# Optimization experiments

Hardware: AMD Instinct MI355X
Metric: run time of the kernel (lower is better)

The kernel has to match this reference:

```python
import jax, jax.numpy as jnp
import numpy as np


def setup_inputs() -> dict:
    key = jax.random.key(0)
    k1, k2, k3, k4 = jax.random.split(key, 4)
    T = 64            # decoder_batch_len (target steps)
    B = 32            # batch_size
    V = 50257         # decoder vocab size
    L = 400           # encoder (source) length
    rows = T * B
    vocab_ds = jax.random.uniform(k1, (rows, V), dtype=jnp.float32)
    attns = jax.random.uniform(k2, (rows, L), dtype=jnp.float32)
    p_gens = jax.random.uniform(k3, (rows, 1), dtype=jnp.float32)
    sources = jax.random.randint(k4, (L, B), 0, V, dtype=jnp.int64)
    return {
        "vocab_ds": vocab_ds,
        "attns": attns,
        "p_gens": p_gens,
        "sources": sources,
        "decoder_batch_len": T,
    }


def reference(vocab_ds, attns, p_gens, sources, decoder_batch_len):
    # vocab_ds: (T*B, V), attns: (T*B, L), p_gens: (T*B, 1), sources: (L, B)
    rows, V = vocab_ds.shape
    vocab_dists = p_gens * vocab_ds                      # gated generation dist
    attn_dists = (1.0 - p_gens) * attns                  # gated copy dist
    # sources.T tiled over decoder steps -> per-row vocab ids, shape (T*B, L)
    sources_rep = jnp.tile(sources.T, (decoder_batch_len, 1))
    row_idx = jnp.arange(rows)[:, None]                  # (T*B, 1) broadcasts over L
    # torch scatter_ (overwrite semantics) of copy probs into vocab slots
    attn_dists_projected = jnp.zeros((rows, V), dtype=vocab_ds.dtype).at[
        row_idx, sources_rep
    ].set(attn_dists, mode="drop")
    final_dists = attn_dists_projected + vocab_dists
    return final_dists
```

## Files before the change

### kernel.cpp

```cpp
#include <hip/hip_runtime.h>

typedef float f32x4 __attribute__((ext_vector_type(4)));
typedef unsigned int uint32;

#define MAXV 51200
#define NWMAX (MAXV / 32 + 1)
#define LPAD 1024

__global__ __launch_bounds__(256) void sort_kernel(
    const int* __restrict__ sources, int* __restrict__ sv, int* __restrict__ sl,
    int L, int B, int V)
{
    const int b = blockIdx.x;
    __shared__ int s_col[LPAD];
    for (int l = threadIdx.x; l < L; l += 256) {
        const int v = sources[(size_t)l * B + b];
        s_col[l] = (v >= 0 && v < V) ? v : 0x7FFFFFFF;
    }
    __syncthreads();
    int* __restrict__ svb = sv + (size_t)b * L;
    int* __restrict__ slb = sl + (size_t)b * L;
    for (int l = threadIdx.x; l < L; l += 256) {
        const int v = s_col[l];
        int rank = 0;
        for (int k = 0; k < L; ++k) {
            const int vk = s_col[k];
            rank += (vk < v) || (vk == v && k < l);
        }
        svb[rank] = v;
        slb[rank] = l;
    }
}

__global__ __launch_bounds__(256) void fused_kernel(
    const float* __restrict__ vd, const float* __restrict__ attns,
    const float* __restrict__ pgs, const int* __restrict__ sv,
    const int* __restrict__ sl, float* __restrict__ out, int V, int L, int B)
{
    const int row = blockIdx.x;
    const int tid = threadIdx.x;
    const int b   = row % B;

    __shared__ uint32 bm[NWMAX];
    __shared__ int    s_v[LPAD];
    __shared__ int    s_l[LPAD];
    __shared__ float  s_attn[LPAD];

    const int NW = (V + 31) >> 5;
    for (int w = tid; w < NW + 1; w += 256) bm[w] = 0u;
    const int* __restrict__ svb = sv + (size_t)b * L;
    const int* __restrict__ slb = sl + (size_t)b * L;
    for (int t = tid; t < LPAD; t += 256) {
        s_v[t]    = (t < L) ? svb[t] : 0x7FFFFFFF;
        s_l[t]    = (t < L) ? slb[t] : 0;
        s_attn[t] = (t < L) ? attns[(size_t)row * L + t] : 0.0f;
    }
    __syncthreads();
    for (int t = tid; t < L; t += 256) {
        const int v = s_v[t];
        if (v < V) atomicOr(&bm[v >> 5], 1u << (v & 31));
    }
    __syncthreads();

    const float pg   = pgs[row];
    const float gate = 1.0f - pg;
    const size_t base = (size_t)row * (size_t)V;

    auto lookup = [&](int j) -> float {
        int lo = 0, hi = LPAD;
        while (lo < hi) {
            const int mid = (lo + hi) >> 1;
            if (s_v[mid] <= j) lo = mid + 1; else hi = mid;
        }
        return gate * s_attn[s_l[lo - 1]];
    };

    const int mis  = (int)(base & 3);
    const int pre  = mis ? (4 - mis) : 0;
    const int preN = pre < V ? pre : V;
    if (tid < preN) {
        const int j = tid;
        float x = pg * vd[base + j];
        if ((bm[j >> 5] >> (j & 31)) & 1u) x += lookup(j);
        __builtin_nontemporal_store(x, &out[base + j]);
    }

    const int nvec = (V - preN) >> 2;
    const f32x4* __restrict__ v4 = (const f32x4*)(vd + base + preN);
    f32x4* __restrict__ o4       = (f32x4*)(out + base + preN);

    auto proc = [&](int i) {
        f32x4 x = v4[i];
        x *= pg;
        const int j0 = preN + (i << 2);
        const int w  = j0 >> 5;
        const uint32 sh = (uint32)(j0 & 31);
        uint32 bits;
        if (sh <= 28u) bits = (bm[w] >> sh) & 0xFu;
        else           bits = ((bm[w] >> sh) | (bm[w + 1] << (32u - sh))) & 0xFu;
        if (bits) {
#pragma unroll
            for (int e = 0; e < 4; ++e)
                if ((bits >> e) & 1u) x[e] += lookup(j0 + e);
        }
        __builtin_nontemporal_store(x, &o4[i]);
    };

    int i = tid;
    for (; i + 768 < nvec; i += 1024) {
        proc(i); proc(i + 256); proc(i + 512); proc(i + 768);
    }
    for (; i < nvec; i += 256) proc(i);

    for (int j = preN + (nvec << 2) + tid; j < V; j += 256) {
        float x = pg * vd[base + j];
        if ((bm[j >> 5] >> (j & 31)) & 1u) x += lookup(j);
        __builtin_nontemporal_store(x, &out[base + j]);
    }
}

__global__ __launch_bounds__(256) void fused_fallback_kernel(
    const float* __restrict__ vocab_ds, const float* __restrict__ attns,
    const float* __restrict__ p_gens, const int* __restrict__ sources,
    float* __restrict__ out, int V, int L, int B)
{
    const int row = blockIdx.x;
    const int tid = threadIdx.x;
    const size_t base = (size_t)row * (size_t)V;
    const float pg = p_gens[row];

    const int mis  = (int)(base & 3);
    const int pre  = mis ? (4 - mis) : 0;
    const int preN = pre < V ? pre : V;
    for (int j = tid; j < preN; j += blockDim.x)
        out[base + j] = pg * vocab_ds[base + j];
    const int nvec = (V - preN) >> 2;
    const f32x4* __restrict__ v4 = (const f32x4*)(vocab_ds + base + preN);
    f32x4* __restrict__ o4       = (f32x4*)(out + base + preN);
    for (int i = tid; i < nvec; i += blockDim.x) {
        f32x4 x = v4[i];
        x *= pg;
        o4[i] = x;
    }
    for (int j = preN + (nvec << 2) + tid; j < V; j += blockDim.x)
        out[base + j] = pg * vocab_ds[base + j];

    __shared__ int s_src[512];
    const int b = row % B;
    const bool use_lds = (L <= 512);
    if (use_lds) {
        for (int l = tid; l < L; l += blockDim.x)
            s_src[l] = sources[(size_t)l * B + b];
    }
    __syncthreads();
    const float gate = 1.0f - pg;
    for (int l = tid; l < L; l += blockDim.x) {
        const int v = use_lds ? s_src[l] : sources[(size_t)l * B + b];
        if (v < 0 || v >= V) continue;
        bool last = true;
        for (int l2 = l + 1; l2 < L; ++l2) {
            const int v2 = use_lds ? s_src[l2] : sources[(size_t)l2 * B + b];
            if (v2 == v) { last = false; break; }
        }
        if (last) {
            const float a = gate * attns[(size_t)row * L + l];
            out[base + v] = pg * vocab_ds[base + v] + a;
        }
    }
}

extern "C" void kernel_launch(void* const* d_in, const int* in_sizes, int n_in,
                              void* d_out, int out_size, void* d_ws, size_t ws_size,
                              hipStream_t stream) {
    const float* vocab_ds = (const float*)d_in[0];
    const float* attns    = (const float*)d_in[1];
    const float* p_gens   = (const float*)d_in[2];
    const int*   sources  = (const int*)d_in[3];
    const int rows = in_sizes[2];
    const int V    = in_sizes[0] / rows;
    const int L    = in_sizes[1] / rows;
    const int B    = in_sizes[3] / L;
    float* out = (float*)d_out;

    const size_t need = (size_t)B * (size_t)L * 2 * sizeof(int);
    const bool fits = (ws_size >= need) && (V <= (NWMAX - 1) * 32) && (L <= LPAD);
    if (fits) {
        int* sv = (int*)d_ws;
        int* sl = sv + (size_t)B * (size_t)L;
        sort_kernel<<<B, 256, 0, stream>>>(sources, sv, sl, L, B, V);
        fused_kernel<<<rows, 256, 0, stream>>>(vocab_ds, attns, p_gens,
                                               sv, sl, out, V, L, B);
    } else {
        fused_fallback_kernel<<<rows, 256, 0, stream>>>(
            vocab_ds, attns, p_gens, sources, out, V, L, B);
    }
}
```

Before: 234.4 us.

## Flatten main kernel into grid-stride loop with global per-batch bitmaps

```diff
diff --git a/kernel.cpp b/kernel.cpp
--- a/kernel.cpp
+++ b/kernel.cpp
@@ -2,22 +2,25 @@
 
 typedef float f32x4 __attribute__((ext_vector_type(4)));
 typedef unsigned int uint32;
-
-#define MAXV 51200
-#define NWMAX (MAXV / 32 + 1)
+typedef unsigned long long uint64;
+
 #define LPAD 1024
 
-__global__ __launch_bounds__(256) void sort_kernel(
+__global__ __launch_bounds__(256) void prep_kernel(
     const int* __restrict__ sources, int* __restrict__ sv, int* __restrict__ sl,
-    int L, int B, int V)
+    uint32* __restrict__ bmG, int L, int B, int V, int NWp)
 {
     const int b = blockIdx.x;
+    uint32* __restrict__ bmb = bmG + (size_t)b * NWp;
+    for (int w = threadIdx.x; w < NWp; w += 256) bmb[w] = 0u;
+
     __shared__ int s_col[LPAD];
     for (int l = threadIdx.x; l < L; l += 256) {
         const int v = sources[(size_t)l * B + b];
         s_col[l] = (v >= 0 && v < V) ? v : 0x7FFFFFFF;
     }
     __syncthreads();
+
     int* __restrict__ svb = sv + (size_t)b * L;
     int* __restrict__ slb = sl + (size_t)b * L;
     for (int l = threadIdx.x; l < L; l += 256) {
@@ -29,93 +32,98 @@
         }
         svb[rank] = v;
         slb[rank] = l;
-    }
-}
-
-__global__ __launch_bounds__(256) void fused_kernel(
+        if (v < V) atomicOr(&bmb[v >> 5], 1u << (v & 31));
+    }
+}
+
+__global__ __launch_bounds__(256) void fused_flat_kernel(
     const float* __restrict__ vd, const float* __restrict__ attns,
     const float* __restrict__ pgs, const int* __restrict__ sv,
-    const int* __restrict__ sl, float* __restrict__ out, int V, int L, int B)
+    const int* __restrict__ sl, const uint32* __restrict__ bmG,
+    float* __restrict__ out, int V, int L, int B, int NWp,
+    uint64 magicM, long long n4, long long total)
 {
-    const int row = blockIdx.x;
-    const int tid = threadIdx.x;
-    const int b   = row % B;
-
-    __shared__ uint32 bm[NWMAX];
-    __shared__ int    s_v[LPAD];
-    __shared__ int    s_l[LPAD];
-    __shared__ float  s_attn[LPAD];
-
-    const int NW = (V + 31) >> 5;
-    for (int w = tid; w < NW + 1; w += 256) bm[w] = 0u;
-    const int* __restrict__ svb = sv + (size_t)b * L;
-    const int* __restrict__ slb = sl + (size_t)b * L;
-    for (int t = tid; t < LPAD; t += 256) {
-        s_v[t]    = (t < L) ? svb[t] : 0x7FFFFFFF;
-        s_l[t]    = (t < L) ? slb[t] : 0;
-        s_attn[t] = (t < L) ? attns[(size_t)row * L + t] : 0.0f;
-    }
-    __syncthreads();
-    for (int t = tid; t < L; t += 256) {
-        const int v = s_v[t];
-        if (v < V) atomicOr(&bm[v >> 5], 1u << (v & 31));
-    }
-    __syncthreads();
-
-    const float pg   = pgs[row];
-    const float gate = 1.0f - pg;
-    const size_t base = (size_t)row * (size_t)V;
-
-    auto lookup = [&](int j) -> float {
-        int lo = 0, hi = LPAD;
-        while (lo < hi) {
-            const int mid = (lo + hi) >> 1;
-            if (s_v[mid] <= j) lo = mid + 1; else hi = mid;
-        }
-        return gate * s_attn[s_l[lo - 1]];
-    };
-
-    const int mis  = (int)(base & 3);
-    const int pre  = mis ? (4 - mis) : 0;
-    const int preN = pre < V ? pre : V;
-    if (tid < preN) {
-        const int j = tid;
-        float x = pg * vd[base + j];
-        if ((bm[j >> 5] >> (j & 31)) & 1u) x += lookup(j);
-        __builtin_nontemporal_store(x, &out[base + j]);
-    }
-
-    const int nvec = (V - preN) >> 2;
-    const f32x4* __restrict__ v4 = (const f32x4*)(vd + base + preN);
-    f32x4* __restrict__ o4       = (f32x4*)(out + base + preN);
-
-    auto proc = [&](int i) {
-        f32x4 x = v4[i];
-        x *= pg;
-        const int j0 = preN + (i << 2);
-        const int w  = j0 >> 5;
-        const uint32 sh = (uint32)(j0 & 31);
-        uint32 bits;
-        if (sh <= 28u) bits = (bm[w] >> sh) & 0xFu;
-        else           bits = ((bm[w] >> sh) | (bm[w + 1] << (32u - sh))) & 0xFu;
-        if (bits) {
+    const long long stride = (long long)gridDim.x * 256;
+    const uint32 bpow2 = ((B & (B - 1)) == 0);
+
+    for (long long i4 = (long long)blockIdx.x * 256 + threadIdx.x;
+         i4 < n4; i4 += stride) {
+        const uint64 g0 = (uint64)i4 << 2;
+        uint32 row = (uint32)((g0 * magicM) >> 48);
+        uint32 j0  = (uint32)(g0 - (uint64)row * (uint32)V);
+        f32x4 x = *(const f32x4*)(vd + g0);
+
+        if (j0 + 4u <= (uint32)V) {
+            const float pg = pgs[row];
+            x *= pg;
+            const uint32 b = bpow2 ? (row & (uint32)(B - 1)) : (row % (uint32)B);
+            const uint32* __restrict__ bmb = bmG + (size_t)b * NWp;
+            const uint32 w = j0 >> 5, sh = j0 & 31u;
+            uint32 bits = bmb[w] >> sh;
+            if (sh > 28u) bits |= bmb[w + 1] << (32u - sh);
+            bits &= 0xFu;
+            if (bits) {
+                const float gate = 1.0f - pg;
+                const int* __restrict__ svb = sv + (size_t)b * L;
+                const int* __restrict__ slb = sl + (size_t)b * L;
 #pragma unroll
-            for (int e = 0; e < 4; ++e)
-                if ((bits >> e) & 1u) x[e] += lookup(j0 + e);
-        }
-        __builtin_nontemporal_store(x, &o4[i]);
-    };
-
-    int i = tid;
-    for (; i + 768 < nvec; i += 1024) {
-        proc(i); proc(i + 256); proc(i + 512); proc(i + 768);
-    }
-    for (; i < nvec; i += 256) proc(i);
-
-    for (int j = preN + (nvec << 2) + tid; j < V; j += 256) {
-        float x = pg * vd[base + j];
-        if ((bm[j >> 5] >> (j & 31)) & 1u) x += lookup(j);
-        __builtin_nontemporal_store(x, &out[base + j]);
+                for (int e = 0; e < 4; ++e)
+                    if ((bits >> e) & 1u) {
+                        const int j = (int)(j0 + e);
+                        int lo = 0, hi = L;
+                        while (lo < hi) {
+                            const int mid = (lo + hi) >> 1;
+                            if (svb[mid] <= j) lo = mid + 1; else hi = mid;
+                        }
+                        x[e] += gate * attns[(size_t)row * L + slb[lo - 1]];
+                    }
+            }
+            __builtin_nontemporal_store(x, (f32x4*)(out + g0));
+        } else {
+            f32x4 xo;
+#pragma unroll
+            for (int e = 0; e < 4; ++e) {
+                uint32 re = row, je = j0 + e;
+                if (je >= (uint32)V) { re = row + 1; je -= (uint32)V; }
+                const float pg = pgs[re];
+                float xe = x[e] * pg;
+                const uint32 b = bpow2 ? (re & (uint32)(B - 1)) : (re % (uint32)B);
+                const uint32* __restrict__ bmb = bmG + (size_t)b * NWp;
+                if ((bmb[je >> 5] >> (je & 31u)) & 1u) {
+                    const int* __restrict__ svb = sv + (size_t)b * L;
+                    const int* __restrict__ slb = sl + (size_t)b * L;
+                    int lo = 0, hi = L;
+                    while (lo < hi) {
+                        const int mid = (lo + hi) >> 1;
+                        if (svb[mid] <= (int)je) lo = mid + 1; else hi = mid;
+                    }
+                    xe += (1.0f - pg) * attns[(size_t)re * L + slb[lo - 1]];
+                }
+                xo[e] = xe;
+            }
+            __builtin_nontemporal_store(xo, (f32x4*)(out + g0));
+        }
+    }
+
+    for (long long g = (n4 << 2) + (long long)blockIdx.x * 256 + threadIdx.x;
+         g < total; g += stride) {
+        const uint32 row = (uint32)(((uint64)g * magicM) >> 48);
+        const uint32 j   = (uint32)((uint64)g - (uint64)row * (uint32)V);
+        const float pg = pgs[row];
+        float xe = pg * vd[g];
+        const uint32 b = bpow2 ? (row & (uint32)(B - 1)) : (row % (uint32)B);
+        const uint32* bmb = bmG + (size_t)b * NWp;
+        if ((bmb[j >> 5] >> (j & 31u)) & 1u) {
+            const int* svb = sv + (size_t)b * L;
+            const int* slb = sl + (size_t)b * L;
+            int lo = 0, hi = L;
+            while (lo < hi) {
+                const int mid = (lo + hi) >> 1;
+                if (svb[mid] <= (int)j) lo = mid + 1; else hi = mid;
+            }
+            xe += (1.0f - pg) * attns[(size_t)row * L + slb[lo - 1]];
+        }
+        __builtin_nontemporal_store(xe, &out[g]);
     }
 }
 
@@ -182,14 +190,25 @@
     const int B    = in_sizes[3] / L;
     float* out = (float*)d_out;
 
-    const size_t need = (size_t)B * (size_t)L * 2 * sizeof(int);
-    const bool fits = (ws_size >= need) && (V <= (NWMAX - 1) * 32) && (L <= LPAD);
+    const int NWp = ((V + 31) >> 5) + 1;
+    const size_t need = (size_t)B * (size_t)L * 2 * sizeof(int)
+                      + (size_t)B * (size_t)NWp * sizeof(uint32);
+    const bool fits = (ws_size >= need) && (L <= LPAD);
+
     if (fits) {
-        int* sv = (int*)d_ws;
-        int* sl = sv + (size_t)B * (size_t)L;
-        sort_kernel<<<B, 256, 0, stream>>>(sources, sv, sl, L, B, V);
-        fused_kernel<<<rows, 256, 0, stream>>>(vocab_ds, attns, p_gens,
-                                               sv, sl, out, V, L, B);
+        int*    sv  = (int*)d_ws;
+        int*    sl  = sv + (size_t)B * (size_t)L;
+        uint32* bmG = (uint32*)(sl + (size_t)B * (size_t)L);
+
+        const long long total = (long long)rows * (long long)V;
+        const long long n4    = total >> 2;
+        const uint64 magicM =
+            (uint64)((((__uint128_t)1) << 48) / (uint32)V) + 1ull;
+
+        prep_kernel<<<B, 256, 0, stream>>>(sources, sv, sl, bmG, L, B, V, NWp);
+        fused_flat_kernel<<<2048, 256, 0, stream>>>(
+            vocab_ds, attns, p_gens, sv, sl, bmG, out,
+            V, L, B, NWp, magicM, n4, total);
     } else {
         fused_fallback_kernel<<<rows, 256, 0, stream>>>(
             vocab_ds, attns, p_gens, sources, out, V, L, B);
```

Measured after the change: 481.7 us. 106% more time.

## Software-pipeline vocab loads with inline-asm loads and explicit vmcnt waits

Applied to the files above, without the earlier changes.

```diff
diff --git a/kernel.cpp b/kernel.cpp
--- a/kernel.cpp
+++ b/kernel.cpp
@@ -89,28 +89,66 @@
     const f32x4* __restrict__ v4 = (const f32x4*)(vd + base + preN);
     f32x4* __restrict__ o4       = (f32x4*)(out + base + preN);
 
-    auto proc = [&](int i) {
-        f32x4 x = v4[i];
+    auto finish = [&](f32x4 x, int i, f32x4* po) {
         x *= pg;
         const int j0 = preN + (i << 2);
         const int w  = j0 >> 5;
         const uint32 sh = (uint32)(j0 & 31);
-        uint32 bits;
-        if (sh <= 28u) bits = (bm[w] >> sh) & 0xFu;
-        else           bits = ((bm[w] >> sh) | (bm[w + 1] << (32u - sh))) & 0xFu;
+        uint32 bits = bm[w] >> sh;
+        if (sh > 28u) bits |= bm[w + 1] << (32u - sh);
+        bits &= 0xFu;
         if (bits) {
 #pragma unroll
             for (int e = 0; e < 4; ++e)
                 if ((bits >> e) & 1u) x[e] += lookup(j0 + e);
         }
-        __builtin_nontemporal_store(x, &o4[i]);
+        __builtin_nontemporal_store(x, po);
     };
 
-    int i = tid;
-    for (; i + 768 < nvec; i += 1024) {
-        proc(i); proc(i + 256); proc(i + 512); proc(i + 768);
-    }
-    for (; i < nvec; i += 256) proc(i);
+    const int nfull  = nvec >> 8;
+    int nppipe = nfull & ~7;
+
+    if (nppipe >= 8) {
+        const f32x4* pl = v4 + tid;
+        f32x4*       po = o4 + tid;
+        int icur = tid;
+        f32x4 x0, x1, x2, x3, x4_, x5, x6, x7;
+
+#define LOADV(xx)                                                         \
+        asm volatile("global_load_dwordx4 %0, %1, off"                    \
+                     : "=&v"(xx) : "v"(pl) : "memory");                   \
+        pl += 256;
+
+#define CONSUME(xx)                                                       \
+        asm volatile("s_waitcnt vmcnt(7)" ::: "memory");                  \
+        __builtin_amdgcn_sched_barrier(0);                                \
+        finish(xx, icur, po);                                             \
+        po += 256; icur += 256;
+
+        LOADV(x0) LOADV(x1) LOADV(x2) LOADV(x3)
+        LOADV(x4_) LOADV(x5) LOADV(x6) LOADV(x7)
+
+        const int trips = nppipe - 8;
+        for (int t = 0; t < trips; t += 8) {
+            CONSUME(x0) LOADV(x0)
+            CONSUME(x1) LOADV(x1)
+            CONSUME(x2) LOADV(x2)
+            CONSUME(x3) LOADV(x3)
+            CONSUME(x4_) LOADV(x4_)
+            CONSUME(x5) LOADV(x5)
+            CONSUME(x6) LOADV(x6)
+            CONSUME(x7) LOADV(x7)
+        }
+        CONSUME(x0) CONSUME(x1) CONSUME(x2) CONSUME(x3)
+        CONSUME(x4_) CONSUME(x5) CONSUME(x6) CONSUME(x7)
+#undef LOADV
+#undef CONSUME
+    } else {
+        nppipe = 0;
+    }
+
+    for (int i = nppipe * 256 + tid; i < nvec; i += 256)
+        finish(v4[i], i, o4 + i);
 
     for (int j = preN + (nvec << 2) + tid; j < V; j += 256) {
         float x = pg * vd[base + j];
```

New measurement: 251.4 us. 1.07x slower.

## Stream vocab rows through LDS with double-buffered global_load_lds pipeline

Applied to the files above, without the earlier changes.

```diff
diff --git a/kernel.cpp b/kernel.cpp
--- a/kernel.cpp
+++ b/kernel.cpp
@@ -2,10 +2,13 @@
 
 typedef float f32x4 __attribute__((ext_vector_type(4)));
 typedef unsigned int uint32;
+typedef unsigned short ushort16;
 
 #define MAXV 51200
 #define NWMAX (MAXV / 32 + 1)
 #define LPAD 1024
+#define LP2 512
+#define WCH 512
 
 __global__ __launch_bounds__(256) void sort_kernel(
     const int* __restrict__ sources, int* __restrict__ sv, int* __restrict__ sl,
@@ -37,28 +40,35 @@
     const float* __restrict__ pgs, const int* __restrict__ sv,
     const int* __restrict__ sl, float* __restrict__ out, int V, int L, int B)
 {
-    const int row = blockIdx.x;
-    const int tid = threadIdx.x;
-    const int b   = row % B;
-
-    __shared__ uint32 bm[NWMAX];
-    __shared__ int    s_v[LPAD];
-    __shared__ int    s_l[LPAD];
-    __shared__ float  s_attn[LPAD];
+    const int row  = blockIdx.x;
+    const int tid  = threadIdx.x;
+    const int wid  = tid >> 6;
+    const int lane = tid & 63;
+    const int b    = row % B;
+
+    __shared__ __align__(16) float stage[4][2][WCH];
+    __shared__ uint32    bm[NWMAX];
+    __shared__ ushort16  s_v[LP2];
+    __shared__ float     s_attn[LP2];
 
     const int NW = (V + 31) >> 5;
     for (int w = tid; w < NW + 1; w += 256) bm[w] = 0u;
     const int* __restrict__ svb = sv + (size_t)b * L;
     const int* __restrict__ slb = sl + (size_t)b * L;
-    for (int t = tid; t < LPAD; t += 256) {
-        s_v[t]    = (t < L) ? svb[t] : 0x7FFFFFFF;
-        s_l[t]    = (t < L) ? slb[t] : 0;
-        s_attn[t] = (t < L) ? attns[(size_t)row * L + t] : 0.0f;
+    for (int t = tid; t < LP2; t += 256) {
+        int v = 0xFFFF; float a = 0.0f;
+        if (t < L) {
+            const int vv = svb[t];
+            v = (vv > 0xFFFF) ? 0xFFFF : vv;
+            a = attns[(size_t)row * L + slb[t]];
+        }
+        s_v[t]    = (ushort16)v;
+        s_attn[t] = a;
     }
     __syncthreads();
     for (int t = tid; t < L; t += 256) {
-        const int v = s_v[t];
-        if (v < V) atomicOr(&bm[v >> 5], 1u << (v & 31));
+        const int v = svb[t];
+        if (v >= 0 && v < V) atomicOr(&bm[v >> 5], 1u << (v & 31));
     }
     __syncthreads();
 
@@ -67,12 +77,27 @@
     const size_t base = (size_t)row * (size_t)V;
 
     auto lookup = [&](int j) -> float {
-        int lo = 0, hi = LPAD;
+        int lo = 0, hi = LP2;
         while (lo < hi) {
             const int mid = (lo + hi) >> 1;
-            if (s_v[mid] <= j) lo = mid + 1; else hi = mid;
-        }
-        return gate * s_attn[s_l[lo - 1]];
+            if ((int)s_v[mid] <= j) lo = mid + 1; else hi = mid;
+        }
+        return gate * s_attn[lo - 1];
+    };
+
+    auto finish = [&](f32x4 x, int j0, f32x4* p) {
+        x *= pg;
+        const int w  = j0 >> 5;
+        const uint32 sh = (uint32)(j0 & 31);
+        uint32 bits = bm[w] >> sh;
+        if (sh > 28u) bits |= bm[w + 1] << (32u - sh);
+        bits &= 0xFu;
+        if (bits) {
+#pragma unroll
+            for (int e = 0; e < 4; ++e)
+                if ((bits >> e) & 1u) x[e] += lookup(j0 + e);
+        }
+        __builtin_nontemporal_store(x, p);
     };
 
     const int mis  = (int)(base & 3);
@@ -85,33 +110,51 @@
         __builtin_nontemporal_store(x, &out[base + j]);
     }
 
-    const int nvec = (V - preN) >> 2;
-    const f32x4* __restrict__ v4 = (const f32x4*)(vd + base + preN);
-    f32x4* __restrict__ o4       = (f32x4*)(out + base + preN);
-
-    auto proc = [&](int i) {
+    const float* rsrc = vd + base + preN;
+    float*       rdst = out + base + preN;
+    const int navail = V - preN;
+    const int nal    = navail & ~(4 * WCH - 1);
+    const int nk     = nal >> 11;
+
+    if (nk > 0) {
+        float* buf0 = &stage[wid][0][0];
+        float* buf1 = &stage[wid][1][0];
+
+        auto issue = [&](float* lbuf, int k, bool real) {
+            const float* g = real ? (rsrc + (((size_t)(k * 4 + wid)) << 9))
+                                  : rsrc;
+            __builtin_amdgcn_global_load_lds(g + (lane << 2),        lbuf,       16, 0, 0);
+            __builtin_amdgcn_global_load_lds(g + (lane << 2) + 256,  lbuf + 256, 16, 0, 0);
+        };
+        auto consume = [&](const float* lbuf, int k) {
+            const int f0 = ((k * 4 + wid) << 9) + (lane << 2);
+            f32x4 x0 = *(const f32x4*)&lbuf[lane << 2];
+            f32x4 x1 = *(const f32x4*)&lbuf[(lane << 2) + 256];
+            finish(x0, preN + f0,       (f32x4*)(rdst + f0));
+            finish(x1, preN + f0 + 256, (f32x4*)(rdst + f0 + 256));
+        };
+
+        issue(buf0, 0, true);
+        issue(buf1, 1, nk > 1);
+        asm volatile("s_waitcnt vmcnt(2)" ::: "memory");
+        __builtin_amdgcn_sched_barrier(0);
+        consume(buf0, 0);
+        for (int k = 1; k < nk; ++k) {
+            float* bufc = (k & 1) ? buf1 : buf0;
+            float* bufn = (k & 1) ? buf0 : buf1;
+            issue(bufn, k + 1, k + 1 < nk);
+            asm volatile("s_waitcnt vmcnt(4)" ::: "memory");
+            __builtin_amdgcn_sched_barrier(0);
+            consume(bufc, k);
+        }
+    }
+
+    const int nvec = navail >> 2;
+    const f32x4* __restrict__ v4 = (const f32x4*)rsrc;
+    for (int i = (nal >> 2) + tid; i < nvec; i += 256) {
         f32x4 x = v4[i];
-        x *= pg;
-        const int j0 = preN + (i << 2);
-        const int w  = j0 >> 5;
-        const uint32 sh = (uint32)(j0 & 31);
-        uint32 bits;
-        if (sh <= 28u) bits = (bm[w] >> sh) & 0xFu;
-        else           bits = ((bm[w] >> sh) | (bm[w + 1] << (32u - sh))) & 0xFu;
-        if (bits) {
-#pragma unroll
-            for (int e = 0; e < 4; ++e)
-                if ((bits >> e) & 1u) x[e] += lookup(j0 + e);
-        }
-        __builtin_nontemporal_store(x, &o4[i]);
-    };
-
-    int i = tid;
-    for (; i + 768 < nvec; i += 1024) {
-        proc(i); proc(i + 256); proc(i + 512); proc(i + 768);
-    }
-    for (; i < nvec; i += 256) proc(i);
-
+        finish(x, preN + (i << 2), (f32x4*)(rdst + (i << 2)));
+    }
     for (int j = preN + (nvec << 2) + tid; j < V; j += 256) {
         float x = pg * vd[base + j];
         if ((bm[j >> 5] >> (j & 31)) & 1u) x += lookup(j);
@@ -183,7 +226,8 @@
     float* out = (float*)d_out;
 
     const size_t need = (size_t)B * (size_t)L * 2 * sizeof(int);
-    const bool fits = (ws_size >= need) && (V <= (NWMAX - 1) * 32) && (L <= LPAD);
+    const bool fits = (ws_size >= need) && (V <= (NWMAX - 1) * 32) &&
+                      (V <= 65534) && (L <= LP2);
     if (fits) {
         int* sv = (int*)d_ws;
         int* sl = sv + (size_t)B * (size_t)L;
```

Measured after the change: 237.9 us. About the same (+1.5%).
